# Performance work log

Measured on AMD Instinct MI355X. Metric: run time of the kernel, lower is better.

Reference implementation:

```python
import jax, jax.numpy as jnp
import numpy as np

NEG = -1e9  # matches self.huge in the torch module


def setup_inputs() -> dict:
    key = jax.random.key(0)
    k1, k2, k3 = jax.random.split(key, 3)
    B, n, nt, t = 64, 50, 30, 60
    S = nt + t
    return {
        "unary_scores": jax.random.normal(k1, (B, n, t), dtype=jnp.float32),
        "rule_scores": jax.random.normal(k2, (B, nt, S, S), dtype=jnp.float32),
        "root_scores": jax.random.normal(k3, (B, nt), dtype=jnp.float32),
        "nt_states": nt,
        "t_states": t,
    }


def _inside(unary_scores, rule_scores, root_scores, nt_states, t_states):
    B, n, _ = unary_scores.shape
    S = nt_states + t_states
    # beta chart [B, n+1, n+1, S]. Width-1 cells hold terminal (preterminal)
    # scores at indices [nt:], all other entries are -huge, exactly as in the
    # torch code. Because invalid children are -huge, summing over ALL S
    # child states with the full rule tensor reproduces the original
    # width-2/3/>=4 case split (tmp1/tmp2/tmp3) exactly.
    beta = jnp.full((B, n + 1, n + 1, S), NEG, dtype=unary_scores.dtype)
    ks = jnp.arange(n)
    beta = beta.at[:, ks, ks + 1, nt_states:].set(unary_scores)

    # stabilized exp of rules, shared across all widths (fast-PCFG style)
    m_rule = rule_scores.max(axis=(2, 3))                      # [B, nt]
    erule = jnp.exp(rule_scores - m_rule[:, :, None, None])    # [B, nt, S, S]

    for w in range(2, n + 1):
        ns = n - w + 1                       # number of start positions
        s_idx = jnp.arange(ns)
        u_idx = s_idx[:, None] + jnp.arange(1, w)[None, :]     # [ns, w-1] split points
        lc = beta[:, s_idx[:, None], u_idx, :]                 # [B, ns, k, S]
        rc = beta[:, u_idx, (s_idx + w)[:, None], :]           # [B, ns, k, S]
        m_l = lc.max(-1)                                       # [B, ns, k]
        m_r = rc.max(-1)
        M = (m_l + m_r).max(-1)                                # [B, ns]
        # fold per-split stabilizer into left child
        el = jnp.exp(lc - m_l[..., None]) * jnp.exp(m_l + m_r - M[..., None])[..., None]
        er = jnp.exp(rc - m_r[..., None])
        # logsumexp over (split k, left l, right r) done as two contractions:
        # new[b,n,p] = log sum_{k,l,r} el*er*erule + M + m_rule
        t1 = jnp.einsum('bnkr,bplr->bnkpl', er, erule)         # [B, ns, k, nt, S]
        ssum = jnp.einsum('bnkpl,bnkl->bnp', t1, el)           # [B, ns, nt]
        new = jnp.log(ssum) + M[:, :, None] + m_rule[:, None, :]
        beta = beta.at[:, s_idx, s_idx + w, :nt_states].set(new)

    log_Z = jax.nn.logsumexp(beta[:, 0, n, :nt_states] + root_scores, axis=1)
    return log_Z


def reference(unary_scores, rule_scores, root_scores, nt_states, t_states):
    return _inside(unary_scores, rule_scores, root_scores, int(nt_states), int(t_states))
```

## Files before the change

### kernel.cpp

```cpp
#include <hip/hip_runtime.h>
#include <hip/hip_bf16.h>

#define NEGF (-1000000000.0f)

namespace {

constexpr int B  = 64;
constexpr int N  = 50;
constexpr int NT = 30;
constexpr int T  = 60;
constexpr int S  = 90;
constexpr int NP1 = N + 1;
constexpr int NSMAX = N - 1;
constexpr int SS = S * S;
constexpr int CELLS = NT * NSMAX;
constexpr int ECOUNT = B * NP1 * NP1 * S;

constexpr int KP  = 96;
constexpr int KK  = S * KP;
constexpr int KSPL = 15;
constexpr int KT2B = 64;
constexpr int NKT = KK / KT2B;
constexpr int TPC = NKT / KSPL;
constexpr int ROWB  = 72;
constexpr int AOFFB = 32 * ROWB;
constexpr int MTOTB = (32 + 64) * ROWB;

constexpr int S1R = 96;
constexpr int S1STR = 72;

using bf16x8 = __attribute__((ext_vector_type(8))) short;
using f32x4  = __attribute__((ext_vector_type(4))) float;

__device__ __forceinline__ unsigned int pk4_e4m3(float a, float b, float c, float d){
  int w = __builtin_amdgcn_cvt_pk_fp8_f32(a, b, 0, false);
  w = __builtin_amdgcn_cvt_pk_fp8_f32(c, d, w, true);
  return (unsigned int)w;
}

__global__ void unary_init(const float* __restrict__ unary,
                           float* __restrict__ mb, short* __restrict__ E){
  int k = blockIdx.x, b = blockIdx.y, j = threadIdx.x;
  float v = (j < T) ? unary[(b*N + k)*T + j] : NEGF;
  float m = v;
  #pragma unroll
  for (int off = 32; off > 0; off >>= 1) m = fmaxf(m, __shfl_xor(m, off));
  if (j == 0) mb[(b*NP1 + k)*NP1 + (k+1)] = m;
  if (j < T){
    __hip_bfloat16 h = __float2bfloat16(__expf(v - m));
    E[((b*NP1 + k)*NP1 + (k+1))*S + NT + j] = *reinterpret_cast<short*>(&h);
  }
}

__global__ __launch_bounds__(256) void rule_prep(const float* __restrict__ rule,
                                                 float* __restrict__ m_rule,
                                                 unsigned char* __restrict__ erule8){
  int p = blockIdx.x, b = blockIdx.y, tid = threadIdx.x;
  size_t base = (size_t)(b*NT + p) * SS;
  size_t obase = (size_t)(b*NT + p) * KK;
  const float4* r4 = (const float4*)(rule + base);
  float lm = NEGF;
  for (int i = tid; i < SS/4; i += 256){
    float4 v = r4[i];
    lm = fmaxf(fmaxf(lm, fmaxf(v.x, v.y)), fmaxf(v.z, v.w));
  }
  #pragma unroll
  for (int off = 32; off > 0; off >>= 1) lm = fmaxf(lm, __shfl_xor(lm, off));
  __shared__ float wmax[4];
  __shared__ float sm;
  if ((tid & 63) == 0) wmax[tid >> 6] = lm;
  __syncthreads();
  if (tid == 0){
    float m = fmaxf(fmaxf(wmax[0], wmax[1]), fmaxf(wmax[2], wmax[3]));
    m_rule[b*NT + p] = m;
    sm = m;
  }
  __syncthreads();
  float m = sm;
  for (int idx = tid; idx < S * 24; idx += 256){
    int l = idx / 24, q4 = idx - l * 24;
    int r = q4 * 4;
    float e[4];
    #pragma unroll
    for (int j = 0; j < 4; ++j){
      int rr = r + j;
      e[j] = (rr < S) ? __expf(rule[base + l*S + rr] - m) : 0.f;
    }
    *(unsigned int*)&erule8[obase + l*KP + r] = pk4_e4m3(e[0], e[1], e[2], e[3]);
  }
}

__global__ __launch_bounds__(256) void stage1(int w, const short* __restrict__ E,
                                              const float* __restrict__ mb,
                                              float* __restrict__ Mbuf,
                                              unsigned char* __restrict__ Og8){
  int s = blockIdx.x, b = blockIdx.y, e = s + w, tid = threadIdx.x;
  int K = w - 1;
  int Kpad = (K + 31) & ~31;
  __shared__ float stmp[NSMAX];
  __shared__ float cK[NSMAX];
  __shared__ float sM;
  __shared__ __align__(16) short sbuf[2 * S1R * S1STR];
  short* elT = sbuf;
  short* erT = sbuf + S1R * S1STR;

  if (tid < K){
    int u = s + tid + 1;
    stmp[tid] = mb[(b*NP1 + s)*NP1 + u] + mb[(b*NP1 + u)*NP1 + e];
  }
  __syncthreads();
  if (tid == 0){
    float M = NEGF;
    for (int k = 0; k < K; ++k) M = fmaxf(M, stmp[k]);
    sM = M;
    Mbuf[b*NSMAX + s] = M;
  }
  __syncthreads();
  float M = sM;
  if (tid < K) cK[tid] = __expf(stmp[tid] - M);
  __syncthreads();

  int items = S1R * Kpad;
  for (int idx = tid; idx < items; idx += 256){
    int k = idx / S1R, i = idx - k * S1R;
    short ve = 0, vr = 0;
    if (i < S && k < K){
      int u = s + k + 1;
      bool lOK = (k == 0)     ? (i >= NT) : (i < NT);
      bool rOK = (k == K - 1) ? (i >= NT) : (i < NT);
      if (lOK){
        unsigned short eL = (unsigned short)E[((b*NP1 + s)*NP1 + u)*S + i];
        float el = __uint_as_float((unsigned int)eL << 16) * cK[k];
        __hip_bfloat16 he = __float2bfloat16(el);
        ve = *reinterpret_cast<short*>(&he);
      }
      if (rOK) vr = E[((b*NP1 + u)*NP1 + e)*S + i];
    }
    elT[i*S1STR + k] = ve;
    erT[i*S1STR + k] = vr;
  }
  __syncthreads();

  int wid = tid >> 6, lane = tid & 63;
  int rr = lane & 15, hi = lane >> 4;
  int ksteps = Kpad >> 5;
  f32x4 accs[9];
  #pragma unroll
  for (int j = 0; j < 9; ++j){
    int t = wid * 9 + j;
    int tr = t / 6, tc = t - tr * 6;
    int ar = tr*16 + rr, br = tc*16 + rr;
    f32x4 acc = {0.f, 0.f, 0.f, 0.f};
    for (int ks = 0; ks < ksteps; ++ks){
      int kb = ks*32 + hi*8;
      bf16x8 af = *(bf16x8*)&elT[ar*S1STR + kb];
      bf16x8 bf2 = *(bf16x8*)&erT[br*S1STR + kb];
      acc = __builtin_amdgcn_mfma_f32_16x16x32_bf16(af, bf2, acc, 0, 0, 0);
    }
    accs[j] = acc;
  }
  __syncthreads();

  unsigned char* rep = (unsigned char*)sbuf;
  for (int idx = tid; idx < S * (KP - S); idx += 256){
    int l = idx / (KP - S), c = idx - l * (KP - S);
    rep[l*KP + S + c] = 0;
  }
  #pragma unroll
  for (int j = 0; j < 9; ++j){
    int t = wid * 9 + j;
    int tr = t / 6, tc = t - tr * 6;
    int rcol = tc*16 + rr;
    if (rcol < S){
      unsigned int pk = pk4_e4m3(accs[j][0], accs[j][1], accs[j][2], accs[j][3]);
      #pragma unroll
      for (int q = 0; q < 4; ++q){
        int l = tr*16 + hi*4 + q;
        if (l < S) rep[l*KP + rcol] = (unsigned char)((pk >> (8*q)) & 0xff);
      }
    }
  }
  __syncthreads();

  size_t obase = ((size_t)(b*NSMAX + s)) * KK;
  uint4* dst = (uint4*)(Og8 + obase);
  const uint4* src = (const uint4*)rep;
  for (int i = tid; i < KK/16; i += 256) dst[i] = src[i];
}

__global__ __launch_bounds__(512) void stage2(int ns, int ntiles,
                                              const unsigned char* __restrict__ erule8,
                                              const unsigned char* __restrict__ Og8,
                                              float* __restrict__ Cpart){
  int kc = blockIdx.x, b = blockIdx.y, tid = threadIdx.x;
  __shared__ __align__(16) unsigned char ldsb[2 * MTOTB];
  int wid = tid >> 6, lane = tid & 63;
  int mt = wid & 1, nt = wid >> 1;
  f32x4 acc = {0.f, 0.f, 0.f, 0.f};

  for (int i = tid; i < 2*MTOTB/4; i += 512) ((unsigned int*)ldsb)[i] = 0;

  int slot = tid & 7;
  int aRow = (tid >> 3) & 31;
  bool aDo = (tid < 256) && (aRow < NT);
  int bRow = tid >> 3;
  bool bDo = bRow < ns;
  const unsigned char* aSrc = erule8 + ((size_t)(b*NT + (aDo ? aRow : 0))) * KK + slot * 8;
  const unsigned char* bSrc = Og8    + ((size_t)(b*NSMAX + (bDo ? bRow : 0))) * KK + slot * 8;
  int aOff = aRow * ROWB + slot * 8;
  int bOff = AOFFB + bRow * ROWB + slot * 8;

  int arow = mt*16 + (lane & 15);
  int brow = nt*16 + (lane & 15);
  int hi = lane >> 4;
  bool active = nt < ntiles;
  int t0 = kc * TPC;

  uint2 ra, rb;
  if (aDo) ra = *(const uint2*)(aSrc + (size_t)t0 * KT2B);
  if (bDo) rb = *(const uint2*)(bSrc + (size_t)t0 * KT2B);
  __syncthreads();

  int cur = 0;
  for (int tt = 0; tt < TPC; ++tt){
    if (aDo) *(uint2*)&ldsb[cur*MTOTB + aOff] = ra;
    if (bDo) *(uint2*)&ldsb[cur*MTOTB + bOff] = rb;
    if (tt + 1 < TPC){
      size_t koff = (size_t)(t0 + tt + 1) * KT2B;
      if (aDo) ra = *(const uint2*)(aSrc + koff);
      if (bDo) rb = *(const uint2*)(bSrc + koff);
    }
    __syncthreads();
    if (active){
      #pragma unroll
      for (int ks = 0; ks < 2; ++ks){
        int sb = ks*4 + hi;
        long af = *(const long*)&ldsb[cur*MTOTB + arow*ROWB + sb*8];
        long bf2 = *(const long*)&ldsb[cur*MTOTB + AOFFB + brow*ROWB + sb*8];
        acc = __builtin_amdgcn_mfma_f32_16x16x32_fp8_fp8(af, bf2, acc, 0, 0, 0);
      }
    }
    cur ^= 1;
  }

  if (active){
    float* cp = Cpart + ((size_t)(kc*B + b)) * CELLS;
    int scol = nt*16 + (lane & 15);
    if (scol < ns){
      #pragma unroll
      for (int r = 0; r < 4; ++r){
        int p = mt*16 + hi*4 + r;
        if (p < NT) cp[p*ns + scol] = acc[r];
      }
    }
  }
}

__global__ __launch_bounds__(256) void finalize(int w, int ns, const float* __restrict__ Cpart,
                                                const float* __restrict__ Mbuf,
                                                const float* __restrict__ m_rule,
                                                float* __restrict__ mb,
                                                short* __restrict__ E){
  int b = blockIdx.x, tid = threadIdx.x;
  __shared__ float q[CELLS];
  __shared__ float smax[NSMAX];
  __shared__ float emr[NT];
  if (tid < NT) emr[tid] = __expf(m_rule[b*NT + tid]);
  __syncthreads();
  for (int cell = tid; cell < NT * ns; cell += 256){
    int p = cell / ns, si = cell - p * ns;
    float sum = 0.f;
    #pragma unroll
    for (int kc = 0; kc < KSPL; ++kc) sum += Cpart[((size_t)(kc*B + b))*CELLS + cell];
    q[si*NT + p] = sum * emr[p];
  }
  __syncthreads();
  if (tid < ns){
    float m = 1e-37f;
    for (int p = 0; p < NT; ++p) m = fmaxf(m, q[tid*NT + p]);
    smax[tid] = m;
    mb[(b*NP1 + tid)*NP1 + (tid + w)] = Mbuf[b*NSMAX + tid] + __logf(m);
  }
  __syncthreads();
  for (int idx = tid; idx < ns * NT; idx += 256){
    int si = idx / NT, p = idx - si * NT;
    __hip_bfloat16 h = __float2bfloat16(q[idx] / smax[si]);
    E[((b*NP1 + si)*NP1 + (si + w))*S + p] = *reinterpret_cast<short*>(&h);
  }
}

__global__ void root_lse(const float* __restrict__ Cpart, const float* __restrict__ Mbuf,
                         const float* __restrict__ m_rule, const float* __restrict__ root,
                         float* __restrict__ out){
  int b = blockIdx.x, j = threadIdx.x;
  float v = NEGF;
  if (j < NT){
    float sum = 0.f;
    #pragma unroll
    for (int q = 0; q < KSPL; ++q)
      sum += Cpart[((size_t)(q*B + b))*CELLS + j];
    v = __logf(fmaxf(sum, 1e-37f)) + Mbuf[b*NSMAX + 0]
      + m_rule[b*NT + j] + root[b*NT + j];
  }
  float m = v;
  #pragma unroll
  for (int off = 32; off > 0; off >>= 1) m = fmaxf(m, __shfl_xor(m, off));
  float ex = __expf(v - m);
  #pragma unroll
  for (int off = 32; off > 0; off >>= 1) ex += __shfl_xor(ex, off);
  if (j == 0) out[b] = __logf(ex) + m;
}

}

extern "C" void kernel_launch(void* const* d_in, const int* in_sizes, int n_in,
                              void* d_out, int out_size, void* d_ws, size_t ws_size,
                              hipStream_t stream){
  (void)in_sizes; (void)n_in; (void)out_size; (void)ws_size;
  const float* unary = (const float*)d_in[0];
  const float* rule  = (const float*)d_in[1];
  const float* root  = (const float*)d_in[2];

  char* ws = (char*)d_ws;
  size_t off = 0;
  auto alloc = [&](size_t bytes) -> void* {
    void* p = ws + off;
    off += (bytes + 255) & ~(size_t)255;
    return p;
  };
  float* mb     = (float*)alloc(sizeof(float) * (size_t)B * NP1 * NP1);
  float* m_rule = (float*)alloc(sizeof(float) * B * NT);
  float* Mbuf   = (float*)alloc(sizeof(float) * B * NSMAX);
  float* Cpart  = (float*)alloc(sizeof(float) * KSPL * B * CELLS);
  short* E      = (short*)alloc(sizeof(short) * (size_t)ECOUNT);
  unsigned char* erule8 = (unsigned char*)alloc((size_t)B * NT * KK);
  unsigned char* Og8    = (unsigned char*)alloc((size_t)B * NSMAX * KK);

  unary_init<<<dim3(N, B), dim3(64), 0, stream>>>(unary, mb, E);
  rule_prep<<<dim3(NT, B), dim3(256), 0, stream>>>(rule, m_rule, erule8);

  for (int w = 2; w <= N; ++w){
    int ns = N - w + 1;
    int ntiles = (ns + 15) >> 4;
    stage1<<<dim3(ns, B), dim3(256), 0, stream>>>(w, E, mb, Mbuf, Og8);
    stage2<<<dim3(KSPL, B), dim3(512), 0, stream>>>(ns, ntiles, erule8, Og8, Cpart);
    if (w < N)
      finalize<<<dim3(B), dim3(256), 0, stream>>>(w, ns, Cpart, Mbuf, m_rule, mb, E);
  }
  root_lse<<<dim3(B), dim3(64), 0, stream>>>(Cpart, Mbuf, m_rule, root, (float*)d_out);
}
```

Before: 1.624 ms.

## Store chart twice (left/right indexed) and parallelize finalize per span

The chart of exponentiated child scores is kept in two copies: one indexed by (start,end) and a transposed one by (end,start). With this, stage1 reads the left and right children of all split points as contiguous rows with paired 32-bit loads instead of scattered 16-bit gathers. The partial-sum buffer is changed to a span-major layout padded to 32 states, so stage2 writes each MFMA accumulator as one vector store. Finalize now launches one 64-thread block per (span, batch) with a wave-level max reduction instead of one block per batch. The cost is double the chart memory and double the writes in unary_init and finalize.

```diff
diff --git a/kernel.cpp b/kernel.cpp
--- a/kernel.cpp
+++ b/kernel.cpp
@@ -13,7 +13,7 @@
 constexpr int NP1 = N + 1;
 constexpr int NSMAX = N - 1;
 constexpr int SS = S * S;
-constexpr int CELLS = NT * NSMAX;
+constexpr int CELLSP = NSMAX * 32 + 32;
 constexpr int ECOUNT = B * NP1 * NP1 * S;
 
 constexpr int KP  = 96;
@@ -38,8 +38,8 @@
   return (unsigned int)w;
 }
 
-__global__ void unary_init(const float* __restrict__ unary,
-                           float* __restrict__ mb, short* __restrict__ E){
+__global__ void unary_init(const float* __restrict__ unary, float* __restrict__ mb,
+                           short* __restrict__ E_L, short* __restrict__ E_R){
   int k = blockIdx.x, b = blockIdx.y, j = threadIdx.x;
   float v = (j < T) ? unary[(b*N + k)*T + j] : NEGF;
   float m = v;
@@ -48,7 +48,9 @@
   if (j == 0) mb[(b*NP1 + k)*NP1 + (k+1)] = m;
   if (j < T){
     __hip_bfloat16 h = __float2bfloat16(__expf(v - m));
-    E[((b*NP1 + k)*NP1 + (k+1))*S + NT + j] = *reinterpret_cast<short*>(&h);
+    short sv = *reinterpret_cast<short*>(&h);
+    E_L[((size_t)((b*NP1 + k)*NP1 + (k+1)))*S + NT + j] = sv;
+    E_R[((size_t)((b*NP1 + (k+1))*NP1 + k))*S + NT + j] = sv;
   }
 }
 
@@ -90,7 +92,8 @@
   }
 }
 
-__global__ __launch_bounds__(256) void stage1(int w, const short* __restrict__ E,
+__global__ __launch_bounds__(256) void stage1(int w, const short* __restrict__ E_L,
+                                              const short* __restrict__ E_R,
                                               const float* __restrict__ mb,
                                               float* __restrict__ Mbuf,
                                               unsigned char* __restrict__ Og8){
@@ -120,24 +123,35 @@
   if (tid < K) cK[tid] = __expf(stmp[tid] - M);
   __syncthreads();
 
-  int items = S1R * Kpad;
+  const short* baseL = E_L + ((size_t)((b*NP1 + s)*NP1 + s + 1)) * S;
+  const short* baseR = E_R + ((size_t)((b*NP1 + e)*NP1 + s + 1)) * S;
+
+  int items = Kpad * 48;
   for (int idx = tid; idx < items; idx += 256){
-    int k = idx / S1R, i = idx - k * S1R;
-    short ve = 0, vr = 0;
-    if (i < S && k < K){
-      int u = s + k + 1;
-      bool lOK = (k == 0)     ? (i >= NT) : (i < NT);
-      bool rOK = (k == K - 1) ? (i >= NT) : (i < NT);
+    int k = idx / 48, j = idx - k * 48;
+    int i = 2 * j;
+    short v0 = 0, v1 = 0, r0 = 0, r1 = 0;
+    if (k < K && j < 45){
+      bool lOK = (k == 0)     ? (j >= 15) : (j < 15);
+      bool rOK = (k == K - 1) ? (j >= 15) : (j < 15);
       if (lOK){
-        unsigned short eL = (unsigned short)E[((b*NP1 + s)*NP1 + u)*S + i];
-        float el = __uint_as_float((unsigned int)eL << 16) * cK[k];
-        __hip_bfloat16 he = __float2bfloat16(el);
-        ve = *reinterpret_cast<short*>(&he);
+        unsigned int L = *(const unsigned int*)(baseL + k*S + i);
+        float f0 = __uint_as_float(L << 16) * cK[k];
+        float f1 = __uint_as_float(L & 0xFFFF0000u) * cK[k];
+        __hip_bfloat16 h0 = __float2bfloat16(f0), h1 = __float2bfloat16(f1);
+        v0 = *reinterpret_cast<short*>(&h0);
+        v1 = *reinterpret_cast<short*>(&h1);
       }
-      if (rOK) vr = E[((b*NP1 + u)*NP1 + e)*S + i];
-    }
-    elT[i*S1STR + k] = ve;
-    erT[i*S1STR + k] = vr;
+      if (rOK){
+        unsigned int R = *(const unsigned int*)(baseR + k*S + i);
+        r0 = (short)(R & 0xFFFFu);
+        r1 = (short)(R >> 16);
+      }
+    }
+    elT[i*S1STR + k]     = v0;
+    elT[(i+1)*S1STR + k] = v1;
+    erT[i*S1STR + k]     = r0;
+    erT[(i+1)*S1STR + k] = r1;
   }
   __syncthreads();
 
@@ -244,48 +258,45 @@
   }
 
   if (active){
-    float* cp = Cpart + ((size_t)(kc*B + b)) * CELLS;
     int scol = nt*16 + (lane & 15);
     if (scol < ns){
-      #pragma unroll
-      for (int r = 0; r < 4; ++r){
-        int p = mt*16 + hi*4 + r;
-        if (p < NT) cp[p*ns + scol] = acc[r];
-      }
-    }
-  }
-}
-
-__global__ __launch_bounds__(256) void finalize(int w, int ns, const float* __restrict__ Cpart,
-                                                const float* __restrict__ Mbuf,
-                                                const float* __restrict__ m_rule,
-                                                float* __restrict__ mb,
-                                                short* __restrict__ E){
-  int b = blockIdx.x, tid = threadIdx.x;
-  __shared__ float q[CELLS];
-  __shared__ float smax[NSMAX];
-  __shared__ float emr[NT];
-  if (tid < NT) emr[tid] = __expf(m_rule[b*NT + tid]);
-  __syncthreads();
-  for (int cell = tid; cell < NT * ns; cell += 256){
-    int p = cell / ns, si = cell - p * ns;
+      int p0 = mt*16 + hi*4;
+      float* cp = Cpart + ((size_t)(kc*B + b)) * CELLSP + scol*32 + p0;
+      *(f32x4*)cp = acc;
+    }
+  }
+}
+
+__global__ __launch_bounds__(64) void finalize(int w, const float* __restrict__ Cpart,
+                                               const float* __restrict__ Mbuf,
+                                               const float* __restrict__ m_rule,
+                                               float* __restrict__ mb,
+                                               short* __restrict__ E_L,
+                                               short* __restrict__ E_R){
+  int sp = blockIdx.x, b = blockIdx.y, tid = threadIdx.x;
+  __shared__ float qs[32];
+  float q = 1e-37f;
+  if (tid < NT){
     float sum = 0.f;
     #pragma unroll
-    for (int kc = 0; kc < KSPL; ++kc) sum += Cpart[((size_t)(kc*B + b))*CELLS + cell];
-    q[si*NT + p] = sum * emr[p];
-  }
-  __syncthreads();
-  if (tid < ns){
-    float m = 1e-37f;
-    for (int p = 0; p < NT; ++p) m = fmaxf(m, q[tid*NT + p]);
-    smax[tid] = m;
-    mb[(b*NP1 + tid)*NP1 + (tid + w)] = Mbuf[b*NSMAX + tid] + __logf(m);
-  }
-  __syncthreads();
-  for (int idx = tid; idx < ns * NT; idx += 256){
-    int si = idx / NT, p = idx - si * NT;
-    __hip_bfloat16 h = __float2bfloat16(q[idx] / smax[si]);
-    E[((b*NP1 + si)*NP1 + (si + w))*S + p] = *reinterpret_cast<short*>(&h);
+    for (int kc = 0; kc < KSPL; ++kc)
+      sum += Cpart[((size_t)(kc*B + b))*CELLSP + sp*32 + tid];
+    q = sum * __expf(m_rule[b*NT + tid]);
+    qs[tid] = q;
+  }
+  float m = (tid < NT) ? q : 1e-37f;
+  #pragma unroll
+  for (int off = 32; off > 0; off >>= 1) m = fmaxf(m, __shfl_xor(m, off));
+  m = fmaxf(m, 1e-37f);
+  __syncthreads();
+  if (tid == 0) mb[(b*NP1 + sp)*NP1 + (sp + w)] = Mbuf[b*NSMAX + sp] + __logf(m);
+  if (tid < 15){
+    float e0 = qs[2*tid] / m, e1 = qs[2*tid + 1] / m;
+    __hip_bfloat16 h0 = __float2bfloat16(e0), h1 = __float2bfloat16(e1);
+    unsigned int pk = (unsigned int)*(unsigned short*)&h0 |
+                      ((unsigned int)*(unsigned short*)&h1 << 16);
+    *(unsigned int*)&E_L[((size_t)((b*NP1 + sp)*NP1 + sp + w))*S + 2*tid] = pk;
+    *(unsigned int*)&E_R[((size_t)((b*NP1 + sp + w)*NP1 + sp))*S + 2*tid] = pk;
   }
 }
 
@@ -298,7 +309,7 @@
     float sum = 0.f;
     #pragma unroll
     for (int q = 0; q < KSPL; ++q)
-      sum += Cpart[((size_t)(q*B + b))*CELLS + j];
+      sum += Cpart[((size_t)(q*B + b))*CELLSP + j];
     v = __logf(fmaxf(sum, 1e-37f)) + Mbuf[b*NSMAX + 0]
       + m_rule[b*NT + j] + root[b*NT + j];
   }
@@ -331,21 +342,22 @@
   float* mb     = (float*)alloc(sizeof(float) * (size_t)B * NP1 * NP1);
   float* m_rule = (float*)alloc(sizeof(float) * B * NT);
   float* Mbuf   = (float*)alloc(sizeof(float) * B * NSMAX);
-  float* Cpart  = (float*)alloc(sizeof(float) * KSPL * B * CELLS);
-  short* E      = (short*)alloc(sizeof(short) * (size_t)ECOUNT);
+  float* Cpart  = (float*)alloc(sizeof(float) * KSPL * B * CELLSP);
+  short* E_L    = (short*)alloc(sizeof(short) * (size_t)ECOUNT);
+  short* E_R    = (short*)alloc(sizeof(short) * (size_t)ECOUNT);
   unsigned char* erule8 = (unsigned char*)alloc((size_t)B * NT * KK);
   unsigned char* Og8    = (unsigned char*)alloc((size_t)B * NSMAX * KK);
 
-  unary_init<<<dim3(N, B), dim3(64), 0, stream>>>(unary, mb, E);
+  unary_init<<<dim3(N, B), dim3(64), 0, stream>>>(unary, mb, E_L, E_R);
   rule_prep<<<dim3(NT, B), dim3(256), 0, stream>>>(rule, m_rule, erule8);
 
   for (int w = 2; w <= N; ++w){
     int ns = N - w + 1;
     int ntiles = (ns + 15) >> 4;
-    stage1<<<dim3(ns, B), dim3(256), 0, stream>>>(w, E, mb, Mbuf, Og8);
+    stage1<<<dim3(ns, B), dim3(256), 0, stream>>>(w, E_L, E_R, mb, Mbuf, Og8);
     stage2<<<dim3(KSPL, B), dim3(512), 0, stream>>>(ns, ntiles, erule8, Og8, Cpart);
     if (w < N)
-      finalize<<<dim3(B), dim3(256), 0, stream>>>(w, ns, Cpart, Mbuf, m_rule, mb, E);
+      finalize<<<dim3(ns, B), dim3(64), 0, stream>>>(w, Cpart, Mbuf, m_rule, mb, E_L, E_R);
   }
   root_lse<<<dim3(B), dim3(64), 0, stream>>>(Cpart, Mbuf, m_rule, root, (float*)d_out);
 }
```

Measured after the change: 1.543 ms. 1.05x faster.
